# Kernel optimization log

Hardware: AMD Instinct MI355X
Metric: run time of the kernel (lower is better)

## Reference

```python
import jax, jax.numpy as jnp
import numpy as np

EPS = 1e-8  # F.cosine_similarity default eps


def setup_inputs() -> dict:
    key = jax.random.key(0)
    k1, k2, k3, k4 = jax.random.split(key, 4)
    N, M, D, BERT_DIM = 8192, 8192, 128, 768
    return {
        "vision_feature": jax.random.normal(k1, (N, D), dtype=jnp.float32),
        "text_pooled": jax.random.normal(k2, (M, BERT_DIM), dtype=jnp.float32),
        "proj_w": jax.random.normal(k3, (D, BERT_DIM), dtype=jnp.float32) * 0.02,
        "proj_b": jax.random.normal(k4, (D,), dtype=jnp.float32) * 0.02,
    }


def reference(vision_feature, text_pooled, proj_w, proj_b):
    # proj(text_pooled): [M, 768] @ [768, D] + [D] -> [M, D]
    text_feature = text_pooled @ proj_w.T + proj_b
    # Fused cosine similarity: L2-normalize rows (with eps clamp as in
    # F.cosine_similarity), then a single [N,D]x[D,M] GEMM instead of the
    # broadcasted O(N*M*D) intermediate.
    v_norm = jnp.maximum(jnp.linalg.norm(vision_feature, axis=1, keepdims=True), EPS)
    t_norm = jnp.maximum(jnp.linalg.norm(text_feature, axis=1, keepdims=True), EPS)
    vn = vision_feature / v_norm  # [N, D]
    tn = text_feature / t_norm    # [M, D]
    similarity = vn @ tn.T        # [N, M]
    return similarity
```

## Files before the change

### kernel.cpp

```cpp
#include <hip/hip_runtime.h>
#include <stdint.h>

#define NV 8192
#define MT 8192
#define DD 128
#define KB 768

typedef __attribute__((ext_vector_type(8))) short short8;
typedef __attribute__((ext_vector_type(4))) float f32x4;

__device__ __forceinline__ ushort f2bf(float f) {
  uint32_t u = __float_as_uint(f);
  u += 0x7FFF + ((u >> 16) & 1);
  return (ushort)(u >> 16);
}

__global__ __launch_bounds__(256) void k_visnorm(const float* __restrict__ vis,
                                                 ushort* __restrict__ vn) {
  const int tx = threadIdx.x & 15;
  const int r  = blockIdx.x * 16 + (threadIdx.x >> 4);
  const float* p = vis + (size_t)r * DD + tx * 8;
  float4 a = *(const float4*)p;
  float4 b = *(const float4*)(p + 4);
  float s = a.x*a.x + a.y*a.y + a.z*a.z + a.w*a.w
          + b.x*b.x + b.y*b.y + b.z*b.z + b.w*b.w;
  s += __shfl_xor(s, 1, 16);
  s += __shfl_xor(s, 2, 16);
  s += __shfl_xor(s, 4, 16);
  s += __shfl_xor(s, 8, 16);
  const float inv = 1.0f / fmaxf(sqrtf(s), 1e-8f);
  union { ushort u[8]; uint4 v; } o;
  o.u[0] = f2bf(a.x * inv); o.u[1] = f2bf(a.y * inv);
  o.u[2] = f2bf(a.z * inv); o.u[3] = f2bf(a.w * inv);
  o.u[4] = f2bf(b.x * inv); o.u[5] = f2bf(b.y * inv);
  o.u[6] = f2bf(b.z * inv); o.u[7] = f2bf(b.w * inv);
  *(uint4*)(vn + (size_t)r * DD + tx * 8) = o.v;
}

__global__ __launch_bounds__(256) void k_cvt(const float* __restrict__ src,
                                             ushort* __restrict__ dst) {
  const size_t i = ((size_t)blockIdx.x * 256 + threadIdx.x) * 8;
  float4 a = *(const float4*)(src + i);
  float4 b = *(const float4*)(src + i + 4);
  union { ushort u[8]; uint4 v; } o;
  o.u[0] = f2bf(a.x); o.u[1] = f2bf(a.y); o.u[2] = f2bf(a.z); o.u[3] = f2bf(a.w);
  o.u[4] = f2bf(b.x); o.u[5] = f2bf(b.y); o.u[6] = f2bf(b.z); o.u[7] = f2bf(b.w);
  *(uint4*)(dst + i) = o.v;
}

__global__ __launch_bounds__(64) void k_projnorm(const float* __restrict__ txt,
                                                 const ushort* __restrict__ wb,
                                                 const float* __restrict__ bias,
                                                 ushort* __restrict__ tn) {
  const int lane = threadIdx.x;
  const int row0 = blockIdx.x * 16;
  const int lrow = lane & 15;
  const int g    = lane >> 4;
  const int koff = g * 8;

  const float*  ap = txt + (size_t)(row0 + lrow) * KB + koff;
  const ushort* bp = wb + (size_t)lrow * KB + koff;

  f32x4 acc[8] = {};

#pragma unroll 4
  for (int ks = 0; ks < KB / 32; ++ks) {
    float4 f0 = *(const float4*)(ap + ks * 32);
    float4 f1 = *(const float4*)(ap + ks * 32 + 4);
    short8 a;
    a[0] = (short)f2bf(f0.x); a[1] = (short)f2bf(f0.y);
    a[2] = (short)f2bf(f0.z); a[3] = (short)f2bf(f0.w);
    a[4] = (short)f2bf(f1.x); a[5] = (short)f2bf(f1.y);
    a[6] = (short)f2bf(f1.z); a[7] = (short)f2bf(f1.w);
#pragma unroll
    for (int n = 0; n < 8; ++n) {
      short8 b = *(const short8*)(bp + (size_t)n * 16 * KB + ks * 32);
      acc[n] = __builtin_amdgcn_mfma_f32_16x16x32_bf16(a, b, acc[n], 0, 0, 0);
    }
  }

#pragma unroll
  for (int n = 0; n < 8; ++n) {
    float bv = bias[n * 16 + lrow];
#pragma unroll
    for (int j = 0; j < 4; ++j) acc[n][j] += bv;
  }
  float s0 = 0.f, s1 = 0.f, s2 = 0.f, s3 = 0.f;
#pragma unroll
  for (int n = 0; n < 8; ++n) {
    s0 += acc[n][0] * acc[n][0];
    s1 += acc[n][1] * acc[n][1];
    s2 += acc[n][2] * acc[n][2];
    s3 += acc[n][3] * acc[n][3];
  }
#pragma unroll
  for (int d = 1; d < 16; d <<= 1) {
    s0 += __shfl_xor(s0, d, 16);
    s1 += __shfl_xor(s1, d, 16);
    s2 += __shfl_xor(s2, d, 16);
    s3 += __shfl_xor(s3, d, 16);
  }
  float inv[4];
  inv[0] = 1.0f / fmaxf(sqrtf(s0), 1e-8f);
  inv[1] = 1.0f / fmaxf(sqrtf(s1), 1e-8f);
  inv[2] = 1.0f / fmaxf(sqrtf(s2), 1e-8f);
  inv[3] = 1.0f / fmaxf(sqrtf(s3), 1e-8f);

#pragma unroll
  for (int n = 0; n < 8; ++n)
#pragma unroll
    for (int j = 0; j < 4; ++j)
      tn[(size_t)(row0 + g * 4 + j) * DD + n * 16 + lrow] = f2bf(acc[n][j] * inv[j]);
}

__global__ __launch_bounds__(512, 2) void k_sim(const ushort* __restrict__ vn,
                                                const ushort* __restrict__ tn,
                                                float* __restrict__ out) {
  __shared__ float lsf[128 * 256];

  const int lin  = blockIdx.x;
  const int nlin = (lin & 7) * 128 + (lin >> 3);
  const int by   = nlin >> 5;
  const int bx   = nlin & 31;
  const int row0 = by * 256;
  const int col0 = bx * 256;

  const int t    = threadIdx.x;
  const int lane = t & 63;
  const int wave = t >> 6;
  const int wr   = wave >> 1;
  const int wc   = wave & 1;
  const int lrow = lane & 15;
  const int kgrp = lane >> 4;

  const ushort* ap = vn + (size_t)(row0 + wr * 64 + lrow) * DD + kgrp * 8;
  const ushort* bp = tn + (size_t)(col0 + wc * 128 + lrow) * DD + kgrp * 8;

  f32x4 acc[4][8] = {};

#pragma unroll
  for (int ks = 0; ks < 4; ++ks) {
    short8 a[4], b[8];
#pragma unroll
    for (int m = 0; m < 4; ++m)
      a[m] = *(const short8*)(ap + (size_t)m * 16 * DD + ks * 32);
#pragma unroll
    for (int n = 0; n < 8; ++n)
      b[n] = *(const short8*)(bp + (size_t)n * 16 * DD + ks * 32);
#pragma unroll
    for (int m = 0; m < 4; ++m)
#pragma unroll
      for (int n = 0; n < 8; ++n)
        acc[m][n] = __builtin_amdgcn_mfma_f32_16x16x32_bf16(a[m], b[n], acc[m][n], 0, 0, 0);
  }

#pragma unroll
  for (int h = 0; h < 2; ++h) {
    __syncthreads();
    if ((wr >> 1) == h) {
      const int rbase = (wr & 1) * 64;
#pragma unroll
      for (int m = 0; m < 4; ++m)
#pragma unroll
        for (int n = 0; n < 8; ++n) {
          const int c = wc * 128 + n * 16 + lrow;
#pragma unroll
          for (int j = 0; j < 4; ++j) {
            const int rl = rbase + m * 16 + kgrp * 4 + j;
            lsf[rl * 256 + (c ^ (((rl >> 2) & 1) << 4))] = acc[m][n][j];
          }
        }
    }
    __syncthreads();
    const f32x4* lsf4 = (const f32x4*)lsf;
#pragma unroll
    for (int p = 0; p < 16; ++p) {
      const int fi = p * 512 + t;
      const int rl = fi >> 6;
      const int c4 = fi & 63;
      f32x4 v = lsf4[rl * 64 + (c4 ^ (((rl >> 2) & 1) << 2))];
      __builtin_nontemporal_store(
          v, (f32x4*)(out + (size_t)(row0 + h * 128 + rl) * MT + col0 + c4 * 4));
    }
  }
}

extern "C" void kernel_launch(void* const* d_in, const int* in_sizes, int n_in,
                              void* d_out, int out_size, void* d_ws, size_t ws_size,
                              hipStream_t stream) {
  (void)in_sizes; (void)n_in; (void)out_size; (void)ws_size;
  const float* vis  = (const float*)d_in[0];
  const float* txt  = (const float*)d_in[1];
  const float* w    = (const float*)d_in[2];
  const float* bias = (const float*)d_in[3];
  float* out = (float*)d_out;

  char* ws = (char*)d_ws;
  ushort* vn = (ushort*)(ws);
  ushort* tn = (ushort*)(ws + (size_t)2097152);
  ushort* wb = (ushort*)(ws + (size_t)4194304);

  k_visnorm<<<NV / 16, 256, 0, stream>>>(vis, vn);
  k_cvt<<<(DD * KB) / 2048, 256, 0, stream>>>(w, wb);
  k_projnorm<<<MT / 16, 64, 0, stream>>>(txt, wb, bias, tn);
  k_sim<<<1024, 512, 0, stream>>>(vn, tn, out);
}
```

Before: 140.8 us.

## Shrink similarity tiles to 128x128 and store MFMA results directly without LDS

The similarity GEMM now uses 256-thread blocks covering 128x128 output tiles with 4096 blocks, each wave computing a 64x64 sub-tile. The LDS staging buffer and its synchronisation-based epilogue are removed, and each lane writes its accumulator scalars straight to global memory with nontemporal stores. This removes the LDS round trip and barriers and raises occupancy. In exchange, each global store is a scalar where the old path wrote 16-byte vectors, so write coalescing may suffer on an output-bandwidth-bound kernel.

New measurement: 137.5 us. -2.3%, faster.

```diff
diff --git a/kernel.cpp b/kernel.cpp
--- a/kernel.cpp
+++ b/kernel.cpp
@@ -113,76 +113,53 @@
       tn[(size_t)(row0 + g * 4 + j) * DD + n * 16 + lrow] = f2bf(acc[n][j] * inv[j]);
 }
 
-__global__ __launch_bounds__(512, 2) void k_sim(const ushort* __restrict__ vn,
+__global__ __launch_bounds__(256, 3) void k_sim(const ushort* __restrict__ vn,
                                                 const ushort* __restrict__ tn,
                                                 float* __restrict__ out) {
-  __shared__ float lsf[128 * 256];
+  const int lin  = blockIdx.x;
+  const int nlin = (lin & 7) * 512 + (lin >> 3);
+  const int by   = nlin >> 6;
+  const int bx   = nlin & 63;
 
-  const int lin  = blockIdx.x;
-  const int nlin = (lin & 7) * 128 + (lin >> 3);
-  const int by   = nlin >> 5;
-  const int bx   = nlin & 31;
-  const int row0 = by * 256;
-  const int col0 = bx * 256;
+  const int lane = threadIdx.x & 63;
+  const int wave = threadIdx.x >> 6;
+  const int row0 = by * 128 + (wave >> 1) * 64;
+  const int col0 = bx * 128 + (wave & 1) * 64;
+  const int lrow = lane & 15;
+  const int koff = (lane >> 4) * 8;
 
-  const int t    = threadIdx.x;
-  const int lane = t & 63;
-  const int wave = t >> 6;
-  const int wr   = wave >> 1;
-  const int wc   = wave & 1;
-  const int lrow = lane & 15;
-  const int kgrp = lane >> 4;
+  const ushort* ap = vn + (size_t)(row0 + lrow) * DD + koff;
+  const ushort* bp = tn + (size_t)(col0 + lrow) * DD + koff;
 
-  const ushort* ap = vn + (size_t)(row0 + wr * 64 + lrow) * DD + kgrp * 8;
-  const ushort* bp = tn + (size_t)(col0 + wc * 128 + lrow) * DD + kgrp * 8;
-
-  f32x4 acc[4][8] = {};
+  f32x4 acc[4][4] = {};
 
 #pragma unroll
   for (int ks = 0; ks < 4; ++ks) {
-    short8 a[4], b[8];
+    short8 a[4], b[4];
 #pragma unroll
     for (int m = 0; m < 4; ++m)
       a[m] = *(const short8*)(ap + (size_t)m * 16 * DD + ks * 32);
 #pragma unroll
-    for (int n = 0; n < 8; ++n)
+    for (int n = 0; n < 4; ++n)
       b[n] = *(const short8*)(bp + (size_t)n * 16 * DD + ks * 32);
 #pragma unroll
     for (int m = 0; m < 4; ++m)
 #pragma unroll
-      for (int n = 0; n < 8; ++n)
+      for (int n = 0; n < 4; ++n)
         acc[m][n] = __builtin_amdgcn_mfma_f32_16x16x32_bf16(a[m], b[n], acc[m][n], 0, 0, 0);
   }
 
+  const int orow = (lane >> 4) * 4;
+  const int ocol = lane & 15;
+  float* op = out + (size_t)(row0 + orow) * MT + col0 + ocol;
 #pragma unroll
-  for (int h = 0; h < 2; ++h) {
-    __syncthreads();
-    if ((wr >> 1) == h) {
-      const int rbase = (wr & 1) * 64;
+  for (int m = 0; m < 4; ++m)
 #pragma unroll
-      for (int m = 0; m < 4; ++m)
+    for (int n = 0; n < 4; ++n)
 #pragma unroll
-        for (int n = 0; n < 8; ++n) {
-          const int c = wc * 128 + n * 16 + lrow;
-#pragma unroll
-          for (int j = 0; j < 4; ++j) {
-            const int rl = rbase + m * 16 + kgrp * 4 + j;
-            lsf[rl * 256 + (c ^ (((rl >> 2) & 1) << 4))] = acc[m][n][j];
-          }
-        }
-    }
-    __syncthreads();
-    const f32x4* lsf4 = (const f32x4*)lsf;
-#pragma unroll
-    for (int p = 0; p < 16; ++p) {
-      const int fi = p * 512 + t;
-      const int rl = fi >> 6;
-      const int c4 = fi & 63;
-      f32x4 v = lsf4[rl * 64 + (c4 ^ (((rl >> 2) & 1) << 2))];
-      __builtin_nontemporal_store(
-          v, (f32x4*)(out + (size_t)(row0 + h * 128 + rl) * MT + col0 + c4 * 4));
-    }
-  }
+      for (int j = 0; j < 4; ++j)
+        __builtin_nontemporal_store(acc[m][n][j],
+                                    op + (size_t)(m * 16 + j) * MT + n * 16);
 }
 
 extern "C" void kernel_launch(void* const* d_in, const int* in_sizes, int n_in,
@@ -203,5 +180,5 @@
   k_visnorm<<<NV / 16, 256, 0, stream>>>(vis, vn);
   k_cvt<<<(DD * KB) / 2048, 256, 0, stream>>>(w, wb);
   k_projnorm<<<MT / 16, 64, 0, stream>>>(txt, wb, bias, tn);
-  k_sim<<<1024, 512, 0, stream>>>(vn, tn, out);
+  k_sim<<<4096, 256, 0, stream>>>(vn, tn, out);
 }
```
